# Kernel tuning notes

Hardware: AMD Instinct MI355X
Metric: run time of the kernel (lower is better)

Reference implementation:

```python
import jax, jax.numpy as jnp
import numpy as np

N_NODES = 50000
N_EDGES = 800000
IN_DIM = 128
HID_DIM = 128
OUT_DIM = 128
THRESH = 0.05
SCALE = 50.0
EPS = 1e-6


def _graph_conv(src, dst, feat, W, b):
    """DGL GraphConv with norm='both': D_out^{-1/2} -> sum-aggregate -> D_in^{-1/2} -> linear."""
    N = feat.shape[0]
    ones = jnp.ones(src.shape[0], feat.dtype)
    deg_out = jax.ops.segment_sum(ones, src, num_segments=N)
    deg_in = jax.ops.segment_sum(ones, dst, num_segments=N)
    norm_src = jax.lax.rsqrt(jnp.maximum(deg_out, 1.0))
    norm_dst = jax.lax.rsqrt(jnp.maximum(deg_in, 1.0))
    h = feat * norm_src[:, None]                       # [N, d]
    agg = jax.ops.segment_sum(h[src], dst, num_segments=N)  # SpMM: gather + scatter-add
    return (agg * norm_dst[:, None]) @ W + b


def _gnn(src, dst, x, W1, b1, W2, b2):
    h = jax.nn.relu(_graph_conv(src, dst, x, W1, b1))
    return _graph_conv(src, dst, h, W2, b2)


def _corr(z1, z2):
    # torch .std uses ddof=1 (unbiased)
    z1s = (z1 - z1.mean(axis=0)) / (jnp.std(z1, axis=0, ddof=1) + EPS)
    z2s = (z2 - z2.mean(axis=0)) / (jnp.std(z2, axis=0, ddof=1) + EPS)
    return (z1s.T @ z2s) / z1.shape[0]


def setup_inputs() -> dict:
    key = jax.random.key(0)
    ks = jax.random.split(key, 8)
    x1 = jax.random.normal(ks[0], (N_NODES, IN_DIM), jnp.float32)
    x2 = jax.random.normal(ks[1], (N_NODES, IN_DIM), jnp.float32)
    src1 = jax.random.randint(ks[2], (N_EDGES,), 0, N_NODES, jnp.int32)
    dst1 = jax.random.randint(ks[3], (N_EDGES,), 0, N_NODES, jnp.int32)
    src2 = jax.random.randint(ks[4], (N_EDGES,), 0, N_NODES, jnp.int32)
    dst2 = jax.random.randint(ks[5], (N_EDGES,), 0, N_NODES, jnp.int32)
    W1 = jax.random.normal(ks[6], (IN_DIM, HID_DIM), jnp.float32) / np.sqrt(IN_DIM)
    W2 = jax.random.normal(ks[7], (HID_DIM, OUT_DIM), jnp.float32) / np.sqrt(HID_DIM)
    return {
        "x1": x1, "x2": x2,
        "src1": src1, "dst1": dst1, "src2": src2, "dst2": dst2,
        "W1": W1, "b1": jnp.zeros((HID_DIM,), jnp.float32),
        "W2": W2, "b2": jnp.zeros((OUT_DIM,), jnp.float32),
        "row_offsets": jnp.zeros((OUT_DIM,), jnp.float32),
        "col_offsets": jnp.zeros((OUT_DIM,), jnp.float32),
    }


def reference(x1, x2, src1, dst1, src2, dst2, W1, b1, W2, b2, row_offsets, col_offsets):
    z1 = _gnn(src1, dst1, x1, W1, b1, W2, b2)
    z2 = _gnn(src2, dst2, x2, W1, b1, W2, b2)
    C = _corr(z1, z2)                                  # [D, D]
    row_score = jnp.abs(C).mean(axis=1)
    col_score = jnp.abs(C).mean(axis=0)
    row_mask = jax.nn.sigmoid(SCALE * (row_score + row_offsets - THRESH))
    col_mask = jax.nn.sigmoid(SCALE * (col_score + col_offsets - THRESH))
    C_masked = C * (row_mask[:, None] * col_mask[None, :])
    return (C_masked, row_mask, col_mask, z1, z2)
```

## Files before the change

### kernel.cpp

```cpp
#include <hip/hip_runtime.h>

#define D 128
#define THRESH 0.05f
#define SCALE 50.0f
#define EPS 1e-6f
#define GP 96
#define CSPLIT 4
#define RPB 544
#define NP2 52224
#define PGRP 24
#define CAP 60
#define PS 2
#define NRANGE 4
#define BB 48
#define RMAX 12500
#define RNGP 12512

typedef __attribute__((ext_vector_type(4))) int i4v;
typedef __attribute__((ext_vector_type(4))) float f4v;
typedef _Float16 h8v __attribute__((ext_vector_type(8)));
typedef _Float16 h4v __attribute__((ext_vector_type(4)));

__device__ inline float4 ntload4(const float* p) {
    f4v v = __builtin_nontemporal_load((const f4v*)p);
    return make_float4(v.x, v.y, v.z, v.w);
}

__device__ inline void decode_grq(int bid, int& g, int& r, int& q) {
    g = bid >= (NRANGE * BB);
    int rem = g ? bid - NRANGE * BB : bid;
    r = rem & (NRANGE - 1);
    q = rem >> 2;
}

__global__ void __launch_bounds__(256) count_kernel(const int* __restrict__ src1,
                                                    const int* __restrict__ dst1,
                                                    const int* __restrict__ src2,
                                                    const int* __restrict__ dst2,
                                                    unsigned int* __restrict__ staging,
                                                    int E, int N) {
    __shared__ unsigned int cnt[RMAX];
    int g, r, q;
    decode_grq(blockIdx.x, g, r, q);
    const int* __restrict__ src = g ? src2 : src1;
    const int* __restrict__ dst = g ? dst2 : dst1;

    int rng = (N + NRANGE - 1) / NRANGE;
    int lo = r * rng;
    int hi = min(N, lo + rng);
    int nr = hi - lo;
    int seg = (E + BB - 1) / BB;
    int s0 = q * seg;
    int s1 = min(E, s0 + seg);
    int tid = threadIdx.x;

    for (int i = tid; i < nr; i += 256) cnt[i] = 0u;
    __syncthreads();

    for (int e = s0 + tid * 4; e < s1; e += 1024) {
        int ss[4], dd[4];
        if (e + 4 <= s1) {
            i4v a = *(const i4v*)(src + e);
            i4v b = *(const i4v*)(dst + e);
            ss[0] = a.x; ss[1] = a.y; ss[2] = a.z; ss[3] = a.w;
            dd[0] = b.x; dd[1] = b.y; dd[2] = b.z; dd[3] = b.w;
        } else {
#pragma unroll
            for (int c = 0; c < 4; ++c) {
                int ee = e + c;
                ss[c] = (ee < s1) ? src[ee] : -1;
                dd[c] = (ee < s1) ? dst[ee] : -1;
            }
        }
#pragma unroll
        for (int c = 0; c < 4; ++c) {
            int s = ss[c], d = dd[c];
            if (s >= lo && s < hi) atomicAdd(&cnt[s - lo], 1u);
            if (d >= lo && d < hi) atomicAdd(&cnt[d - lo], 0x10000u);
        }
    }
    __syncthreads();

    unsigned int* row = staging + (size_t)(((g * NRANGE + r) * BB) + q) * RNGP;
    for (int i = tid; i < nr; i += 256) row[i] = cnt[i];
}

__global__ void scan_kernel(unsigned int* __restrict__ staging, int* __restrict__ pad1,
                            int* __restrict__ pad2, int N) {
    int t = blockIdx.x * 256 + threadIdx.x;
    if (t >= 2 * N) return;
    int g = t >= N;
    int d = g ? t - N : t;
    int rng = (N + NRANGE - 1) / NRANGE;
    int r = d / rng;
    int i = d - r * rng;
    int* __restrict__ pad = g ? pad2 : pad1;

    unsigned int* base = staging + (size_t)((g * NRANGE + r) * BB) * RNGP + i;
    unsigned int oc = 0, run = 0;
#pragma unroll 4
    for (int q = 0; q < BB; ++q) {
        unsigned int c = base[(size_t)q * RNGP];
        base[(size_t)q * RNGP] = run;
        oc += c & 0xFFFFu;
        run += c >> 16;
    }
    pad[d * PS] = (int)oc;
    pad[d * PS + 1] = (int)run;
}

__global__ void __launch_bounds__(256) place_kernel(const int* __restrict__ src1,
                                                    const int* __restrict__ dst1,
                                                    const int* __restrict__ src2,
                                                    const int* __restrict__ dst2,
                                                    const unsigned int* __restrict__ staging,
                                                    unsigned short* __restrict__ bucket1,
                                                    unsigned short* __restrict__ bucket2,
                                                    int E, int N) {
    __shared__ unsigned int cur[RMAX];
    int g, r, q;
    decode_grq(blockIdx.x, g, r, q);
    const int* __restrict__ src = g ? src2 : src1;
    const int* __restrict__ dst = g ? dst2 : dst1;
    unsigned short* __restrict__ bucket = g ? bucket2 : bucket1;

    int rng = (N + NRANGE - 1) / NRANGE;
    int lo = r * rng;
    int hi = min(N, lo + rng);
    int nr = hi - lo;
    int seg = (E + BB - 1) / BB;
    int s0 = q * seg;
    int s1 = min(E, s0 + seg);
    int tid = threadIdx.x;

    const unsigned int* row = staging + (size_t)(((g * NRANGE + r) * BB) + q) * RNGP;
    for (int i = tid; i < nr; i += 256) cur[i] = row[i];
    __syncthreads();

    for (int e = s0 + tid * 4; e < s1; e += 1024) {
        int ss[4], dd[4];
        if (e + 4 <= s1) {
            i4v a = *(const i4v*)(src + e);
            i4v b = *(const i4v*)(dst + e);
            ss[0] = a.x; ss[1] = a.y; ss[2] = a.z; ss[3] = a.w;
            dd[0] = b.x; dd[1] = b.y; dd[2] = b.z; dd[3] = b.w;
        } else {
#pragma unroll
            for (int c = 0; c < 4; ++c) {
                int ee = e + c;
                ss[c] = (ee < s1) ? src[ee] : -1;
                dd[c] = (ee < s1) ? dst[ee] : -1;
            }
        }
#pragma unroll
        for (int c = 0; c < 4; ++c) {
            int s = ss[c], d = dd[c];
            if (d >= lo && d < hi) {
                unsigned int pos = atomicAdd(&cur[d - lo], 1u);
                if (pos < CAP) bucket[(size_t)d * CAP + pos] = (unsigned short)s;
            }
        }
    }
}

__global__ void wtrans_kernel(const float* __restrict__ W1, const float* __restrict__ W2,
                              _Float16* __restrict__ Wt1, _Float16* __restrict__ Wt2) {
    int e = blockIdx.x * 256 + threadIdx.x;
    int h = e >= D * D;
    int rem = h ? e - D * D : e;
    int j = rem >> 7, k = rem & 127;
    const float* W = h ? W2 : W1;
    _Float16* Wt = h ? Wt2 : Wt1;
    Wt[j * D + k] = (_Float16)W[k * D + j];
}

template <bool F32IN>
__global__ void __launch_bounds__(256) gemm_ns(const float* __restrict__ tf,
                                               const _Float16* __restrict__ th,
                                               const int* __restrict__ pad,
                                               const _Float16* __restrict__ Wt,
                                               _Float16* __restrict__ y, int N) {
    __shared__ _Float16 sA[128 * D];
    __shared__ _Float16 sB[D * D];
    int tid = threadIdx.x;
    int row0 = blockIdx.x * 128;

#pragma unroll
    for (int q = 0; q < 8; ++q) {
        int c = q * 256 + tid;
        int j = c >> 4, u = c & 15;
        h8v v = *(const h8v*)(Wt + j * D + u * 8);
        int byte = j * 256 + ((u * 16) ^ ((j & 7) << 4));
        *(h8v*)((char*)sB + byte) = v;
    }
#pragma unroll
    for (int q = 0; q < 8; ++q) {
        int c = q * 256 + tid;
        int row = c >> 4, u = c & 15;
        int gr = row0 + row;
        h8v hv = {};
        if (gr < N) {
            if (F32IN) {
                float nsv = rsqrtf(fmaxf((float)pad[gr * PS], 1.f));
                const float* p = tf + (size_t)gr * D + u * 8;
                float4 v0 = *(const float4*)p;
                float4 v1 = *(const float4*)(p + 4);
                hv[0] = (_Float16)(v0.x * nsv); hv[1] = (_Float16)(v0.y * nsv);
                hv[2] = (_Float16)(v0.z * nsv); hv[3] = (_Float16)(v0.w * nsv);
                hv[4] = (_Float16)(v1.x * nsv); hv[5] = (_Float16)(v1.y * nsv);
                hv[6] = (_Float16)(v1.z * nsv); hv[7] = (_Float16)(v1.w * nsv);
            } else {
                hv = *(const h8v*)(th + (size_t)gr * D + u * 8);
            }
        }
        int byte = row * 256 + ((u * 16) ^ ((row & 7) << 4));
        *(h8v*)((char*)sA + byte) = hv;
    }
    __syncthreads();

    int w = tid >> 6;
    int l = tid & 63;
    int l16 = l & 15, lg = l >> 4;
    f4v acc[2][8];
#pragma unroll
    for (int m = 0; m < 2; ++m)
#pragma unroll
        for (int n = 0; n < 8; ++n) acc[m][n] = (f4v){0.f, 0.f, 0.f, 0.f};

#pragma unroll
    for (int kc = 0; kc < 4; ++kc) {
        h8v a[2];
#pragma unroll
        for (int m = 0; m < 2; ++m) {
            int row = w * 32 + m * 16 + l16;
            int u = kc * 4 + lg;
            int byte = row * 256 + ((u * 16) ^ ((row & 7) << 4));
            a[m] = *(const h8v*)((const char*)sA + byte);
        }
#pragma unroll
        for (int n = 0; n < 8; ++n) {
            int j = n * 16 + l16;
            int u = kc * 4 + lg;
            int byte = j * 256 + ((u * 16) ^ ((j & 7) << 4));
            h8v b = *(const h8v*)((const char*)sB + byte);
#pragma unroll
            for (int m = 0; m < 2; ++m)
                acc[m][n] = __builtin_amdgcn_mfma_f32_16x16x32_f16(a[m], b, acc[m][n], 0, 0, 0);
        }
    }

#pragma unroll
    for (int m = 0; m < 2; ++m) {
        int rbase = row0 + w * 32 + m * 16 + lg * 4;
#pragma unroll
        for (int n = 0; n < 8; ++n) {
            int col = n * 16 + l16;
#pragma unroll
            for (int r = 0; r < 4; ++r) {
                int row = rbase + r;
                if (row < N) y[(size_t)row * D + col] = (_Float16)acc[m][n][r];
            }
        }
    }
}

template <bool OUT16>
__global__ void gather_kernel(const unsigned short* __restrict__ bucket,
                              const int* __restrict__ pad, const _Float16* __restrict__ y,
                              const float* __restrict__ bias, float* __restrict__ zf,
                              _Float16* __restrict__ zh, int N) {
    int wave = threadIdx.x >> 6;
    int lane = threadIdx.x & 63;
    int node = blockIdx.x * 4 + wave;
    if (node >= N) return;
    int deg = pad[node * PS + 1];
    int cnt = min(deg, CAP);
    float ndv = rsqrtf(fmaxf((float)deg, 1.f));
    int sid = 0;
    if (lane < cnt) sid = bucket[(size_t)node * CAP + lane];
    int grp = lane >> 4;
    int sl = lane & 15;
    const _Float16* yp = y + sl * 8;
    float acc[8] = {0.f, 0.f, 0.f, 0.f, 0.f, 0.f, 0.f, 0.f};
    for (int j = 0; j < cnt; j += 16) {
        h8v v[4];
        float vw[4];
#pragma unroll
        for (int c = 0; c < 4; ++c) {
            int idx = j + c * 4 + grp;
            int s = __shfl(sid, idx & 63);
            vw[c] = (idx < cnt) ? 1.f : 0.f;
            v[c] = *(const h8v*)(yp + (size_t)s * D);
        }
#pragma unroll
        for (int c = 0; c < 4; ++c)
#pragma unroll
            for (int u = 0; u < 8; ++u)
                acc[u] += (float)v[c][u] * vw[c];
    }
#pragma unroll
    for (int u = 0; u < 8; ++u) {
        acc[u] += __shfl_xor(acc[u], 16);
        acc[u] += __shfl_xor(acc[u], 32);
    }
    if (grp == 0) {
        float4 b0 = *(const float4*)(bias + sl * 8);
        float4 b1 = *(const float4*)(bias + sl * 8 + 4);
        float o[8];
        o[0] = acc[0] * ndv + b0.x; o[1] = acc[1] * ndv + b0.y;
        o[2] = acc[2] * ndv + b0.z; o[3] = acc[3] * ndv + b0.w;
        o[4] = acc[4] * ndv + b1.x; o[5] = acc[5] * ndv + b1.y;
        o[6] = acc[6] * ndv + b1.z; o[7] = acc[7] * ndv + b1.w;
        if (OUT16) {
            float nsv = rsqrtf(fmaxf((float)pad[node * PS], 1.f));
            h8v hv;
#pragma unroll
            for (int u = 0; u < 8; ++u) hv[u] = (_Float16)(fmaxf(o[u], 0.f) * nsv);
            *(h8v*)(zh + (size_t)node * D + sl * 8) = hv;
        } else {
            *(float4*)(zf + (size_t)node * D + sl * 8) = make_float4(o[0], o[1], o[2], o[3]);
            *(float4*)(zf + (size_t)node * D + sl * 8 + 4) = make_float4(o[4], o[5], o[6], o[7]);
        }
    }
}

__global__ void __launch_bounds__(256) ztrans_kernel(const float* __restrict__ z1,
                                                     const float* __restrict__ z2,
                                                     _Float16* __restrict__ zt1,
                                                     _Float16* __restrict__ zt2, int N) {
    __shared__ _Float16 tile[64][132];
    int g = blockIdx.y;
    const float* z = g ? z2 : z1;
    _Float16* zt = g ? zt2 : zt1;
    int n0 = blockIdx.x * 64;
    int tid = threadIdx.x;
#pragma unroll
    for (int it = 0; it < 8; ++it) {
        int idx = it * 256 + tid;
        int row = idx >> 5;
        int c4 = (idx & 31) * 4;
        int gr = n0 + row;
        float4 v = make_float4(0.f, 0.f, 0.f, 0.f);
        if (gr < N) v = *(const float4*)&z[(size_t)gr * D + c4];
        h4v h = {(_Float16)v.x, (_Float16)v.y, (_Float16)v.z, (_Float16)v.w};
        *(h4v*)&tile[row][c4] = h;
    }
    __syncthreads();
    int col = tid >> 1, half = tid & 1;
    _Float16 buf[32];
#pragma unroll
    for (int k = 0; k < 32; ++k) buf[k] = tile[half * 32 + k][col];
    _Float16* dst = zt + (size_t)col * NP2 + n0 + half * 32;
#pragma unroll
    for (int c = 0; c < 4; ++c) *(h8v*)(dst + c * 8) = *(const h8v*)&buf[c * 8];
}

__global__ void __launch_bounds__(512) gram_mfma(const _Float16* __restrict__ zt1,
                                                 const _Float16* __restrict__ zt2,
                                                 float* __restrict__ part,
                                                 float* __restrict__ statpart) {
    int tid = threadIdx.x;
    int w = tid >> 6, l = tid & 63;
    int l16 = l & 15, lg = l >> 4;
    int cy = blockIdx.y * 32;
    f4v acc[2];
    acc[0] = (f4v){0.f, 0.f, 0.f, 0.f};
    acc[1] = (f4v){0.f, 0.f, 0.f, 0.f};
    float sA = 0.f, qA = 0.f, sB = 0.f, qB = 0.f;
    int r0 = blockIdx.x * RPB;
    const _Float16* ap = zt1 + (size_t)(w * 16 + l16) * NP2 + lg * 8;
    const _Float16* bp0 = zt2 + (size_t)(cy + l16) * NP2 + lg * 8;
    const _Float16* bp1 = zt2 + (size_t)(cy + 16 + l16) * NP2 + lg * 8;
#pragma unroll 1
    for (int ks = 0; ks < RPB / 32; ++ks) {
        int k0 = r0 + ks * 32;
        h8v a = *(const h8v*)(ap + k0);
        h8v b0 = *(const h8v*)(bp0 + k0);
        h8v b1 = *(const h8v*)(bp1 + k0);
        if (blockIdx.y == 0) {
#pragma unroll
            for (int j = 0; j < 8; ++j) {
                float f = (float)a[j];
                sA += f;
                qA += f * f;
            }
        }
        if (w < 2) {
            h8v bb = w ? b1 : b0;
#pragma unroll
            for (int j = 0; j < 8; ++j) {
                float f = (float)bb[j];
                sB += f;
                qB += f * f;
            }
        }
        acc[0] = __builtin_amdgcn_mfma_f32_16x16x32_f16(a, b0, acc[0], 0, 0, 0);
        acc[1] = __builtin_amdgcn_mfma_f32_16x16x32_f16(a, b1, acc[1], 0, 0, 0);
    }
    float* pb = part + (size_t)blockIdx.x * (D * D);
#pragma unroll
    for (int n = 0; n < 2; ++n)
#pragma unroll
        for (int r = 0; r < 4; ++r)
            pb[(w * 16 + lg * 4 + r) * D + cy + n * 16 + l16] = acc[n][r];
    float* sp = statpart + (size_t)blockIdx.x * 512;
    if (blockIdx.y == 0) {
        sA += __shfl_xor(sA, 16); sA += __shfl_xor(sA, 32);
        qA += __shfl_xor(qA, 16); qA += __shfl_xor(qA, 32);
        if (lg == 0) {
            int row = w * 16 + l16;
            sp[row] = sA;
            sp[D + row] = qA;
        }
    }
    if (w < 2) {
        sB += __shfl_xor(sB, 16); sB += __shfl_xor(sB, 32);
        qB += __shfl_xor(qB, 16); qB += __shfl_xor(qB, 32);
        if (lg == 0) {
            int col = cy + w * 16 + l16;
            sp[2 * D + col] = sB;
            sp[3 * D + col] = qB;
        }
    }
}

__global__ void reduce_part(const float* __restrict__ part, float* __restrict__ Csum) {
    int e = blockIdx.x * 256 + threadIdx.x;
    int p0 = blockIdx.y * PGRP;
    float s = 0.f;
#pragma unroll
    for (int p = 0; p < PGRP; ++p)
        s += __builtin_nontemporal_load(&part[(size_t)(p0 + p) * (D * D) + e]);
    atomicAdd(&Csum[e], s);
}

__global__ void __launch_bounds__(1024) corrmask_kernel(const float* __restrict__ Csum,
                                                        const float* __restrict__ statpart,
                                                        const float* __restrict__ roff,
                                                        const float* __restrict__ coff,
                                                        float* __restrict__ out, int N) {
    __shared__ float cL[D * D];
    __shared__ float statsh[512];
    __shared__ float m1s[D], i1s[D], m2s[D], i2s[D];
    __shared__ float rowpart[D][2];
    __shared__ float colpart[8][D];
    __shared__ float rms[D], cms[D];
    int t = threadIdx.x;
    int j = t & 127, rg = t >> 7;
    if (t < 512) {
        float s = 0.f;
        for (int p = 0; p < GP; ++p) s += statpart[(size_t)p * 512 + t];
        statsh[t] = s;
    }
    __syncthreads();
    float fn = (float)N;
    if (t < D) {
        float m1 = statsh[t] / fn;
        float v1 = fmaxf((statsh[D + t] - fn * m1 * m1) / (fn - 1.f), 0.f);
        m1s[t] = m1;
        i1s[t] = 1.f / (sqrtf(v1) + EPS);
    } else if (t < 2 * D) {
        int jj = t - D;
        float m2 = statsh[2 * D + jj] / fn;
        float v2 = fmaxf((statsh[3 * D + jj] - fn * m2 * m2) / (fn - 1.f), 0.f);
        m2s[jj] = m2;
        i2s[jj] = 1.f / (sqrtf(v2) + EPS);
    }
    __syncthreads();
    float b = m2s[j], vj = i2s[j];
    float invfn = 1.f / fn;
    float colacc = 0.f;
    for (int k = 0; k < 16; ++k) {
        int i = rg * 16 + k;
        int e = i * D + j;
        float c = (Csum[e] - fn * m1s[i] * b) * (i1s[i] * vj) * invfn;
        cL[e] = c;
        float a = fabsf(c);
        colacc += a;
        for (int o = 1; o < 64; o <<= 1) a += __shfl_xor(a, o);
        if ((j & 63) == 0) rowpart[i][j >> 6] = a;
    }
    colpart[rg][j] = colacc;
    __syncthreads();
    if (t < D) {
        float rs = rowpart[t][0] + rowpart[t][1];
        float rm = 1.f / (1.f + expf(-SCALE * (rs / (float)D + roff[t] - THRESH)));
        rms[t] = rm;
        out[D * D + t] = rm;
    } else if (t < 2 * D) {
        int jj = t - D;
        float cs = 0.f;
#pragma unroll
        for (int g2 = 0; g2 < 8; ++g2) cs += colpart[g2][jj];
        float cm = 1.f / (1.f + expf(-SCALE * (cs / (float)D + coff[jj] - THRESH)));
        cms[jj] = cm;
        out[D * D + D + jj] = cm;
    }
    __syncthreads();
    for (int k = 0; k < 16; ++k) {
        int i = rg * 16 + k;
        int e = i * D + j;
        out[e] = cL[e] * rms[i] * cms[j];
    }
}

extern "C" void kernel_launch(void* const* d_in, const int* in_sizes, int n_in,
                              void* d_out, int out_size, void* d_ws, size_t ws_size,
                              hipStream_t stream) {
    const float* x1 = (const float*)d_in[0];
    const float* x2 = (const float*)d_in[1];
    const int* src1 = (const int*)d_in[2];
    const int* dst1 = (const int*)d_in[3];
    const int* src2 = (const int*)d_in[4];
    const int* dst2 = (const int*)d_in[5];
    const float* W1 = (const float*)d_in[6];
    const float* b1 = (const float*)d_in[7];
    const float* W2 = (const float*)d_in[8];
    const float* b2 = (const float*)d_in[9];
    const float* roff = (const float*)d_in[10];
    const float* coff = (const float*)d_in[11];

    const int N = in_sizes[0] / D;
    const int E = in_sizes[2];

    float* ws = (float*)d_ws;
    unsigned int* staging = (unsigned int*)ws;
    _Float16* y = (_Float16*)ws;
    unsigned short* bucket1 =
        (unsigned short*)(staging + (size_t)2 * NRANGE * BB * RNGP);
    unsigned short* bucket2 = bucket1 + (size_t)N * CAP;
    int* pad1 = (int*)(bucket2 + (size_t)N * CAP);
    int* pad2 = pad1 + (size_t)N * PS;
    _Float16* Wt1 = (_Float16*)(pad2 + (size_t)N * PS);
    _Float16* Wt2 = Wt1 + D * D;
    _Float16* zt1 = (_Float16*)ws;
    _Float16* zt2 = zt1 + (size_t)D * NP2;
    float* part = (float*)(zt2 + (size_t)D * NP2);
    float* Csum = part + (size_t)GP * D * D;
    float* statpart = Csum + D * D;

    float* out = (float*)d_out;
    float* z1 = out + D * D + 2 * D;
    float* z2 = z1 + (size_t)N * D;

    count_kernel<<<2 * NRANGE * BB, 256, 0, stream>>>(src1, dst1, src2, dst2, staging, E, N);
    scan_kernel<<<(2 * N + 255) / 256, 256, 0, stream>>>(staging, pad1, pad2, N);
    place_kernel<<<2 * NRANGE * BB, 256, 0, stream>>>(src1, dst1, src2, dst2, staging,
                                                      bucket1, bucket2, E, N);
    wtrans_kernel<<<2 * D * D / 256, 256, 0, stream>>>(W1, W2, Wt1, Wt2);

    const int gblk = (N + 127) / 128;
    for (int g = 0; g < 2; ++g) {
        const float* x = g ? x2 : x1;
        float* z = g ? z2 : z1;
        _Float16* hp = (_Float16*)z;
        int* pad = g ? pad2 : pad1;
        unsigned short* bucket = g ? bucket2 : bucket1;

        gemm_ns<true><<<gblk, 256, 0, stream>>>(x, nullptr, pad, Wt1, y, N);
        gather_kernel<true><<<(N + 3) / 4, 256, 0, stream>>>(bucket, pad, y, b1, nullptr, hp, N);
        gemm_ns<false><<<gblk, 256, 0, stream>>>(nullptr, hp, pad, Wt2, y, N);
        gather_kernel<false><<<(N + 3) / 4, 256, 0, stream>>>(bucket, pad, y, b2, z, nullptr, N);
    }

    hipMemsetAsync(Csum, 0, sizeof(float) * D * D, stream);
    {
        dim3 tgrid(NP2 / 64, 2);
        ztrans_kernel<<<tgrid, 256, 0, stream>>>(z1, z2, zt1, zt2, N);
    }
    {
        dim3 ggrid(GP, CSPLIT);
        gram_mfma<<<ggrid, 512, 0, stream>>>(zt1, zt2, part, statpart);
    }
    {
        dim3 grid(64, GP / PGRP);
        reduce_part<<<grid, 256, 0, stream>>>(part, Csum);
    }
    corrmask_kernel<<<1, 1024, 0, stream>>>(Csum, statpart, roff, coff, out, N);
}
```

Before: 280.8 us.

## Batch both graph views into single launches and halve gram partitions

The GEMM and gather kernels now take both views' pointers and select one by blockIdx.y, so the two graphs are handled in one launch per stage instead of eight sequential launches. Each view gets its own y buffer so the two can run side by side. The gram kernel uses 48 partitions of 1088 rows instead of 96 of 544, and reduce_part sums all partitions directly instead of using atomics, which removes the memset. This cuts launch count and fills the GPU better for the small kernels, at the cost of extra workspace and a less parallel final reduction.

```diff
diff --git a/kernel.cpp b/kernel.cpp
--- a/kernel.cpp
+++ b/kernel.cpp
@@ -4,11 +4,10 @@
 #define THRESH 0.05f
 #define SCALE 50.0f
 #define EPS 1e-6f
-#define GP 96
+#define GP 48
 #define CSPLIT 4
-#define RPB 544
+#define RPB 1088
 #define NP2 52224
-#define PGRP 24
 #define CAP 60
 #define PS 2
 #define NRANGE 4
@@ -175,13 +174,22 @@
 }
 
 template <bool F32IN>
-__global__ void __launch_bounds__(256) gemm_ns(const float* __restrict__ tf,
-                                               const _Float16* __restrict__ th,
-                                               const int* __restrict__ pad,
+__global__ void __launch_bounds__(256) gemm_ns(const float* __restrict__ tf1,
+                                               const float* __restrict__ tf2,
+                                               const _Float16* __restrict__ th1,
+                                               const _Float16* __restrict__ th2,
+                                               const int* __restrict__ pad1,
+                                               const int* __restrict__ pad2,
                                                const _Float16* __restrict__ Wt,
-                                               _Float16* __restrict__ y, int N) {
+                                               _Float16* __restrict__ y1,
+                                               _Float16* __restrict__ y2, int N) {
     __shared__ _Float16 sA[128 * D];
     __shared__ _Float16 sB[D * D];
+    int g = blockIdx.y;
+    const float* tf = g ? tf2 : tf1;
+    const _Float16* th = g ? th2 : th1;
+    const int* pad = g ? pad2 : pad1;
+    _Float16* y = g ? y2 : y1;
     int tid = threadIdx.x;
     int row0 = blockIdx.x * 128;
 
@@ -265,10 +273,20 @@
 }
 
 template <bool OUT16>
-__global__ void gather_kernel(const unsigned short* __restrict__ bucket,
-                              const int* __restrict__ pad, const _Float16* __restrict__ y,
-                              const float* __restrict__ bias, float* __restrict__ zf,
-                              _Float16* __restrict__ zh, int N) {
+__global__ void gather_kernel(const unsigned short* __restrict__ bucket1,
+                              const unsigned short* __restrict__ bucket2,
+                              const int* __restrict__ pad1, const int* __restrict__ pad2,
+                              const _Float16* __restrict__ y1, const _Float16* __restrict__ y2,
+                              const float* __restrict__ bias,
+                              float* __restrict__ zf1, float* __restrict__ zf2,
+                              _Float16* __restrict__ zh1, _Float16* __restrict__ zh2, int N) {
+    int g = blockIdx.y;
+    const unsigned short* bucket = g ? bucket2 : bucket1;
+    const int* pad = g ? pad2 : pad1;
+    const _Float16* y = g ? y2 : y1;
+    float* zf = g ? zf2 : zf1;
+    _Float16* zh = g ? zh2 : zh1;
+
     int wave = threadIdx.x >> 6;
     int lane = threadIdx.x & 63;
     int node = blockIdx.x * 4 + wave;
@@ -426,12 +444,11 @@
 
 __global__ void reduce_part(const float* __restrict__ part, float* __restrict__ Csum) {
     int e = blockIdx.x * 256 + threadIdx.x;
-    int p0 = blockIdx.y * PGRP;
     float s = 0.f;
-#pragma unroll
-    for (int p = 0; p < PGRP; ++p)
-        s += __builtin_nontemporal_load(&part[(size_t)(p0 + p) * (D * D) + e]);
-    atomicAdd(&Csum[e], s);
+#pragma unroll 8
+    for (int p = 0; p < GP; ++p)
+        s += __builtin_nontemporal_load(&part[(size_t)p * (D * D) + e]);
+    Csum[e] = s;
 }
 
 __global__ void __launch_bounds__(1024) corrmask_kernel(const float* __restrict__ Csum,
@@ -525,7 +542,6 @@
 
     float* ws = (float*)d_ws;
     unsigned int* staging = (unsigned int*)ws;
-    _Float16* y = (_Float16*)ws;
     unsigned short* bucket1 =
         (unsigned short*)(staging + (size_t)2 * NRANGE * BB * RNGP);
     unsigned short* bucket2 = bucket1 + (size_t)N * CAP;
@@ -533,6 +549,8 @@
     int* pad2 = pad1 + (size_t)N * PS;
     _Float16* Wt1 = (_Float16*)(pad2 + (size_t)N * PS);
     _Float16* Wt2 = Wt1 + D * D;
+    _Float16* y1 = Wt2 + D * D;
+    _Float16* y2 = y1 + (size_t)N * D;
     _Float16* zt1 = (_Float16*)ws;
     _Float16* zt2 = zt1 + (size_t)D * NP2;
     float* part = (float*)(zt2 + (size_t)D * NP2);
@@ -542,6 +560,8 @@
     float* out = (float*)d_out;
     float* z1 = out + D * D + 2 * D;
     float* z2 = z1 + (size_t)N * D;
+    _Float16* hp1 = (_Float16*)z1;
+    _Float16* hp2 = (_Float16*)z2;
 
     count_kernel<<<2 * NRANGE * BB, 256, 0, stream>>>(src1, dst1, src2, dst2, staging, E, N);
     scan_kernel<<<(2 * N + 255) / 256, 256, 0, stream>>>(staging, pad1, pad2, N);
@@ -550,20 +570,18 @@
     wtrans_kernel<<<2 * D * D / 256, 256, 0, stream>>>(W1, W2, Wt1, Wt2);
 
     const int gblk = (N + 127) / 128;
-    for (int g = 0; g < 2; ++g) {
-        const float* x = g ? x2 : x1;
-        float* z = g ? z2 : z1;
-        _Float16* hp = (_Float16*)z;
-        int* pad = g ? pad2 : pad1;
-        unsigned short* bucket = g ? bucket2 : bucket1;
-
-        gemm_ns<true><<<gblk, 256, 0, stream>>>(x, nullptr, pad, Wt1, y, N);
-        gather_kernel<true><<<(N + 3) / 4, 256, 0, stream>>>(bucket, pad, y, b1, nullptr, hp, N);
-        gemm_ns<false><<<gblk, 256, 0, stream>>>(nullptr, hp, pad, Wt2, y, N);
-        gather_kernel<false><<<(N + 3) / 4, 256, 0, stream>>>(bucket, pad, y, b2, z, nullptr, N);
-    }
-
-    hipMemsetAsync(Csum, 0, sizeof(float) * D * D, stream);
+    {
+        dim3 gg(gblk, 2), ga((N + 3) / 4, 2);
+        gemm_ns<true><<<gg, 256, 0, stream>>>(x1, x2, nullptr, nullptr, pad1, pad2,
+                                              Wt1, y1, y2, N);
+        gather_kernel<true><<<ga, 256, 0, stream>>>(bucket1, bucket2, pad1, pad2, y1, y2,
+                                                    b1, nullptr, nullptr, hp1, hp2, N);
+        gemm_ns<false><<<gg, 256, 0, stream>>>(nullptr, nullptr, hp1, hp2, pad1, pad2,
+                                               Wt2, y1, y2, N);
+        gather_kernel<false><<<ga, 256, 0, stream>>>(bucket1, bucket2, pad1, pad2, y1, y2,
+                                                     b2, z1, z2, nullptr, nullptr, N);
+    }
+
     {
         dim3 tgrid(NP2 / 64, 2);
         ztrans_kernel<<<tgrid, 256, 0, stream>>>(z1, z2, zt1, zt2, N);
@@ -572,9 +590,6 @@
         dim3 ggrid(GP, CSPLIT);
         gram_mfma<<<ggrid, 512, 0, stream>>>(zt1, zt2, part, statpart);
     }
-    {
-        dim3 grid(64, GP / PGRP);
-        reduce_part<<<grid, 256, 0, stream>>>(part, Csum);
-    }
+    reduce_part<<<64, 256, 0, stream>>>(part, Csum);
     corrmask_kernel<<<1, 1024, 0, stream>>>(Csum, statpart, roff, coff, out, N);
 }
```

Measured after the change: 256.6 us. -8.6%, faster.
